# Optimization experiments

Measured on AMD Instinct MI355X. Metric: run time of the kernel, lower is better.

The kernel has to match this reference:

```python
import jax, jax.numpy as jnp
import numpy as np

B, T, C = 8, 2048, 1024
NEG_BIG = -1e30  # exp(NEG_BIG - row_max) underflows to exactly 0 in fp32


def setup_inputs() -> dict:
    key = jax.random.key(0)
    k1, k2 = jax.random.split(key)
    x = jax.random.normal(k1, (B, T, C), dtype=jnp.float32)
    # nn.Linear weight, shape [out, in]; forward computes x @ W^T
    W_H = jax.random.normal(k2, (C, C), dtype=jnp.float32) * (1.0 / np.sqrt(C))
    return {"x": x, "W_H": W_H}


def reference(x, W_H):
    Tdim = x.shape[1]
    xH = jnp.einsum('btc,dc->btd', x, W_H)          # H(x) = x @ W^T, [B,T,C]
    scores = jnp.einsum('btc,bsc->bts', x, xH)       # bilinear scores, [B,T,T]
    # tril_plus_one=True -> strictly-lower-triangular mask (diagonal=-1)
    mask = jnp.tril(jnp.ones((Tdim, Tdim), dtype=bool), k=-1)
    scores = jnp.where(mask, scores, NEG_BIG)
    wei = jax.nn.softmax(scores, axis=-1)            # fully-masked rows -> uniform, zeroed below
    all_masked = ~mask.any(axis=-1)                  # [T], True for row 0
    wei = jnp.where(all_masked[None, :, None], 0.0, wei)
    out = jnp.einsum('bts,bsc->btc', wei, xH)
    return -out
```

## Files before the change

### kernel.cpp

```cpp
#include <hip/hip_runtime.h>
#include <stdint.h>

#define Bn 8
#define Tn 2048
#define Cn 1024
#define Mn (Bn * Tn)
#define NTRI 136
#define NLIN2 72

typedef __attribute__((ext_vector_type(4))) float f32x4;
typedef _Float16 f16;
typedef __attribute__((ext_vector_type(8))) _Float16 f16x8;
typedef uint16_t u16;
typedef uint32_t u32;

static __device__ __forceinline__ u16 f2h(float f) {
  union { f16 h; u16 u; } c; c.h = (f16)f; return c.u;
}
static __device__ __forceinline__ f32x4 mfmaH(f16x8 a, f16x8 b, f32x4 c) {
  return __builtin_amdgcn_mfma_f32_16x16x32_f16(a, b, c, 0, 0, 0);
}
static __device__ __forceinline__ void gld16(const void* g, void* l) {
  __builtin_amdgcn_global_load_lds(
      (const __attribute__((address_space(1))) u32*)g,
      (__attribute__((address_space(3))) u32*)l, 16, 0, 0);
}

__global__ __launch_bounds__(256) void ksplitW(const float* __restrict__ s,
                                               u16* __restrict__ hi) {
  size_t i = ((size_t)blockIdx.x * 256 + threadIdx.x) * 8;
  float4 a = *(const float4*)(s + i), b = *(const float4*)(s + i + 4);
  float f[8] = {a.x, a.y, a.z, a.w, b.x, b.y, b.z, b.w};
  union { u16 u[8]; uint4 v; } H;
#pragma unroll
  for (int j = 0; j < 8; ++j) H.u[j] = f2h(f[j]);
  *(uint4*)(hi + i) = H.v;
}

__global__ __launch_bounds__(256) void ksplitX(const float* __restrict__ s,
                                               u16* __restrict__ hi,
                                               u16* __restrict__ lo) {
  size_t i = ((size_t)blockIdx.x * 256 + threadIdx.x) * 8;
  float4 a = *(const float4*)(s + i), b = *(const float4*)(s + i + 4);
  float f[8] = {a.x, a.y, a.z, a.w, b.x, b.y, b.z, b.w};
  union { u16 u[8]; uint4 v; } H, L;
#pragma unroll
  for (int j = 0; j < 8; ++j) {
    f16 h = (f16)f[j];
    union { f16 h; u16 u; } ch; ch.h = h;
    H.u[j] = ch.u;
    L.u[j] = f2h(f[j] - (float)h);
  }
  *(uint4*)(hi + i) = H.v;
  *(uint4*)(lo + i) = L.v;
}

__global__ __launch_bounds__(256) void k1_xh(const u16* __restrict__ x_h,
                                             const u16* __restrict__ W_h,
                                             u16* __restrict__ xh) {
  __shared__ __align__(16) u16 Ah[8192], Bh[8192];
  const int tid = threadIdx.x;
  const int m0 = blockIdx.x * 128, n0 = blockIdx.y * 128;
  const int wave = tid >> 6, lane = tid & 63;
  const int wrow = (wave >> 1) * 64, wcol = (wave & 1) * 64;
  const int quad = lane >> 4, l16 = lane & 15;

  f32x4 acc[4][4] = {};

  for (int k0 = 0; k0 < Cn; k0 += 64) {
#pragma unroll
    for (int i = 0; i < 4; ++i) {
      int chunk = i * 256 + tid;
      int kk = chunk >> 9, row = (chunk >> 2) & 127, c8 = (chunk & 3) * 8;
      gld16(x_h + (size_t)(m0 + row) * Cn + k0 + kk * 32 + c8, Ah + chunk * 8);
      gld16(W_h + (size_t)(n0 + row) * Cn + k0 + kk * 32 + c8, Bh + chunk * 8);
    }
    __syncthreads();
#pragma unroll
    for (int kk = 0; kk < 2; ++kk) {
      f16x8 a[4], b[4];
#pragma unroll
      for (int i = 0; i < 4; ++i) {
        a[i] = *(const f16x8*)(Ah + kk * 4096 + (wrow + i * 16 + l16) * 32 + quad * 8);
        b[i] = *(const f16x8*)(Bh + kk * 4096 + (wcol + i * 16 + l16) * 32 + quad * 8);
      }
#pragma unroll
      for (int mi = 0; mi < 4; ++mi)
#pragma unroll
        for (int ni = 0; ni < 4; ++ni)
          acc[mi][ni] = mfmaH(a[mi], b[ni], acc[mi][ni]);
    }
    __syncthreads();
  }
#pragma unroll
  for (int mi = 0; mi < 4; ++mi)
#pragma unroll
    for (int ni = 0; ni < 4; ++ni)
#pragma unroll
      for (int r = 0; r < 4; ++r) {
        int row = wrow + mi * 16 + quad * 4 + r;
        int col = wcol + ni * 16 + l16;
        xh[(size_t)(m0 + row) * Cn + n0 + col] = f2h(acc[mi][ni][r]);
      }
}

__global__ __launch_bounds__(512) void k2_scores(const u16* __restrict__ x_h,
                                                 const u16* __restrict__ x_l,
                                                 const u16* __restrict__ xh,
                                                 u16* __restrict__ P,
                                                 float* __restrict__ mt,
                                                 float* __restrict__ lt) {
  __shared__ __align__(16) union {
    struct { u16 Ah[3][4096], Al[3][4096], Bh[3][8192]; } s;
    struct { float Mrow[4][128]; float Lrow[4][128]; } e;
  } u;
  const int tid = threadIdx.x;
  const int bL = blockIdx.y;
  const int lin = blockIdx.x;
  int qt = 0, cum = 0;
  while (cum + ((qt >> 1) + 1) <= lin) { cum += (qt >> 1) + 1; qt++; }
  const int bcol = lin - cum;
  const int t0 = qt * 128, s0 = bcol * 256;
  const int wave = tid >> 6, lane = tid & 63;
  const int wc = wave & 3;
  const int wrow = (wave >> 2) * 64, wcol = wc * 64;
  const int quad = lane >> 4, l16 = lane & 15;

  f32x4 acc[4][4] = {};
  const size_t abase = ((size_t)bL * Tn + t0) * Cn;
  const size_t bbase = ((size_t)bL * Tn + s0) * Cn;
  const int arow = tid >> 2, ac8 = (tid & 3) * 8;

  auto stage = [&](int buf, int k0) {
    size_t aoff = abase + (size_t)arow * Cn + k0 + ac8;
    gld16(x_h + aoff, &u.s.Ah[buf][tid * 8]);
    gld16(x_l + aoff, &u.s.Al[buf][tid * 8]);
#pragma unroll
    for (int i = 0; i < 2; ++i) {
      int ch = i * 512 + tid;
      int row = ch >> 2, c8 = (ch & 3) * 8;
      gld16(xh + bbase + (size_t)row * Cn + k0 + c8, &u.s.Bh[buf][ch * 8]);
    }
  };

  stage(0, 0);
  stage(1, 32);
  int cur = 0;
#pragma unroll 1
  for (int kidx = 0; kidx < 32; ++kidx) {
    if (kidx < 31) {
      asm volatile("s_waitcnt vmcnt(4) lgkmcnt(0)" ::: "memory");
    } else {
      asm volatile("s_waitcnt vmcnt(0) lgkmcnt(0)" ::: "memory");
    }
    __builtin_amdgcn_s_barrier();
    __builtin_amdgcn_sched_barrier(0);
    if (kidx < 30) {
      int tgt = cur >= 1 ? cur - 1 : 2;
      stage(tgt, (kidx + 2) * 32);
    }
    f16x8 b[4];
#pragma unroll
    for (int ni = 0; ni < 4; ++ni)
      b[ni] = *(const f16x8*)&u.s.Bh[cur][(wcol + ni * 16 + l16) * 32 + quad * 8];
#pragma unroll
    for (int mi = 0; mi < 4; ++mi) {
      f16x8 ah = *(const f16x8*)&u.s.Ah[cur][(wrow + mi * 16 + l16) * 32 + quad * 8];
      f16x8 al = *(const f16x8*)&u.s.Al[cur][(wrow + mi * 16 + l16) * 32 + quad * 8];
#pragma unroll
      for (int ni = 0; ni < 4; ++ni) {
        acc[mi][ni] = mfmaH(ah, b[ni], acc[mi][ni]);
        acc[mi][ni] = mfmaH(al, b[ni], acc[mi][ni]);
      }
    }
    cur = cur < 2 ? cur + 1 : 0;
  }

  float rm[4][4];
#pragma unroll
  for (int mi = 0; mi < 4; ++mi)
#pragma unroll
    for (int r = 0; r < 4; ++r) {
      int row = wrow + mi * 16 + quad * 4 + r;
      float m = -1e30f;
#pragma unroll
      for (int ni = 0; ni < 4; ++ni) {
        int scol = s0 + wcol + ni * 16 + l16;
        if (scol >= t0 + row) acc[mi][ni][r] = -1e30f;
        m = fmaxf(m, acc[mi][ni][r]);
      }
      m = fmaxf(m, __shfl_xor(m, 1));
      m = fmaxf(m, __shfl_xor(m, 2));
      m = fmaxf(m, __shfl_xor(m, 4));
      m = fmaxf(m, __shfl_xor(m, 8));
      rm[mi][r] = m;
    }
  if (l16 == 0) {
#pragma unroll
    for (int mi = 0; mi < 4; ++mi)
#pragma unroll
      for (int r = 0; r < 4; ++r)
        u.e.Mrow[wc][wrow + mi * 16 + quad * 4 + r] = rm[mi][r];
  }
  __syncthreads();
  const int h2 = (wc >> 1) * 2;
  float rs[4][4];
#pragma unroll
  for (int mi = 0; mi < 4; ++mi)
#pragma unroll
    for (int r = 0; r < 4; ++r) {
      int row = wrow + mi * 16 + quad * 4 + r;
      float m2 = fmaxf(u.e.Mrow[h2][row], u.e.Mrow[h2 + 1][row]);
      float s = 0.f;
#pragma unroll
      for (int ni = 0; ni < 4; ++ni) {
        int scol = s0 + wcol + ni * 16 + l16;
        float p = (scol < t0 + row) ? __expf(acc[mi][ni][r] - m2) : 0.0f;
        acc[mi][ni][r] = p;
        s += p;
      }
      s += __shfl_xor(s, 1);
      s += __shfl_xor(s, 2);
      s += __shfl_xor(s, 4);
      s += __shfl_xor(s, 8);
      rs[mi][r] = s;
      rm[mi][r] = m2;
    }
  if (l16 == 0) {
#pragma unroll
    for (int mi = 0; mi < 4; ++mi)
#pragma unroll
      for (int r = 0; r < 4; ++r)
        u.e.Lrow[wc][wrow + mi * 16 + quad * 4 + r] = rs[mi][r];
  }
  __syncthreads();
  const int st128 = bcol * 2 + (wc >> 1);
  if (st128 <= qt) {
    if ((wc & 1) == 0 && l16 == 0) {
#pragma unroll
      for (int mi = 0; mi < 4; ++mi)
#pragma unroll
        for (int r = 0; r < 4; ++r) {
          int row = wrow + mi * 16 + quad * 4 + r;
          size_t rI = (size_t)bL * Tn + t0 + row;
          mt[rI * 16 + st128] = rm[mi][r];
          lt[rI * 16 + st128] = u.e.Lrow[wc][row] + u.e.Lrow[wc + 1][row];
        }
    }
    const size_t pbase = (size_t)(bL * NTRI + qt * (qt + 1) / 2 + st128) * 16384;
#pragma unroll
    for (int mi = 0; mi < 4; ++mi)
#pragma unroll
      for (int ni = 0; ni < 4; ++ni)
#pragma unroll
        for (int r = 0; r < 4; ++r) {
          int row = wrow + mi * 16 + quad * 4 + r;
          int pcol = (wcol & 64) + ni * 16 + l16;
          P[pbase + row * 128 + pcol] = f2h(acc[mi][ni][r]);
        }
  }
}

__global__ __launch_bounds__(256) void k3_stats(const float* __restrict__ mt,
                                                const float* __restrict__ lt,
                                                float* __restrict__ Mr,
                                                float* __restrict__ Li) {
  int r = blockIdx.x * 256 + threadIdx.x;
  int t = r & (Tn - 1);
  int nt = (t == 0) ? 0 : (((t - 1) >> 7) + 1);
  float M = -1e30f;
  for (int i = 0; i < nt; ++i) M = fmaxf(M, mt[(size_t)r * 16 + i]);
  float L = 0.f;
  for (int i = 0; i < nt; ++i) L += lt[(size_t)r * 16 + i] * __expf(mt[(size_t)r * 16 + i] - M);
  Mr[r] = M;
  Li[r] = (L > 0.f) ? 1.f / L : 0.f;
}

__global__ __launch_bounds__(256) void ktr(const u16* __restrict__ src,
                                           u16* __restrict__ dst) {
  __shared__ __align__(16) u16 S[128 * 136];
  const int t0 = blockIdx.x * 128, c0 = blockIdx.y * 128, b = blockIdx.z;
  const int tid = threadIdx.x;
#pragma unroll
  for (int i = 0; i < 8; ++i) {
    int chunk = tid + i * 256;
    int row = chunk >> 4, c8 = (chunk & 15) * 8;
    uint4 v = *(const uint4*)(src + ((size_t)b * Tn + t0 + row) * Cn + c0 + c8);
    *(uint4*)(S + row * 136 + c8) = v;
  }
  __syncthreads();
#pragma unroll
  for (int i = 0; i < 8; ++i) {
    int chunk = tid + i * 256;
    int crow = chunk >> 4, t8 = (chunk & 15) * 8;
    union { u16 s[8]; uint4 v; } o;
#pragma unroll
    for (int j = 0; j < 8; ++j) o.s[j] = S[(t8 + j) * 136 + crow];
    *(uint4*)(dst + ((size_t)b * Cn + c0 + crow) * Tn + t0 + t8) = o.v;
  }
}

__global__ __launch_bounds__(512) void k4_out(const u16* __restrict__ P,
                                              const u16* __restrict__ xhT,
                                              const float* __restrict__ mt,
                                              const float* __restrict__ Mr,
                                              const float* __restrict__ Li,
                                              float* __restrict__ out) {
  __shared__ __align__(16) u16 Ap[3][4096], Bp[3][8192];
  __shared__ u16 alphaLds[16 * 128];
  const int tid = threadIdx.x;
  const int tt = 15 - blockIdx.x;
  const int cn = blockIdx.y, bL = blockIdx.z;
  const int t0 = tt * 128, c0 = cn * 256;
  const int wave = tid >> 6, lane = tid & 63;
  const int wc = wave & 3;
  const int wrow = (wave >> 2) * 64, wcol = wc * 64;
  const int quad = lane >> 4, l16 = lane & 15;

  {
    const size_t rbase = (size_t)bL * Tn + t0;
#pragma unroll
    for (int j = 0; j < 4; ++j) {
      int idx = tid + j * 512;
      int stp = idx >> 7, row = idx & 127;
      float a = 0.f;
      if (stp <= tt)
        a = __expf(mt[(rbase + row) * 16 + stp] - Mr[rbase + row]) * Li[rbase + row];
      alphaLds[idx] = f2h(a);
    }
  }

  f32x4 acc[4][4] = {};
  const size_t bbase = ((size_t)bL * Cn + c0) * Tn;
  const size_t ptile0 = (size_t)(bL * NTRI + tt * (tt + 1) / 2) * 16384;

  auto stage = [&](int buf, int step) {
    const int st = step >> 2, k32 = (step & 3) * 32;
    {
      int row = tid >> 2, c8 = (tid & 3) * 8;
      gld16(P + ptile0 + (size_t)st * 16384 + row * 128 + k32 + c8,
            &Ap[buf][tid * 8]);
    }
#pragma unroll
    for (int i = 0; i < 2; ++i) {
      int ch = i * 512 + tid;
      int row = ch >> 2, c8 = (ch & 3) * 8;
      gld16(xhT + bbase + (size_t)row * Tn + st * 128 + k32 + c8,
            &Bp[buf][ch * 8]);
    }
  };

  const int steps = 4 * (tt + 1);
  stage(0, 0);
  stage(1, 1);
  int cur = 0;
#pragma unroll 1
  for (int s = 0; s < steps; ++s) {
    if (s < steps - 1) {
      asm volatile("s_waitcnt vmcnt(3) lgkmcnt(0)" ::: "memory");
    } else {
      asm volatile("s_waitcnt vmcnt(0) lgkmcnt(0)" ::: "memory");
    }
    __builtin_amdgcn_s_barrier();
    __builtin_amdgcn_sched_barrier(0);
    if (s < steps - 2) {
      int tgt = cur >= 1 ? cur - 1 : 2;
      stage(tgt, s + 2);
    }
    const int st = s >> 2;
    f16x8 b[4];
#pragma unroll
    for (int ni = 0; ni < 4; ++ni)
      b[ni] = *(const f16x8*)&Bp[cur][(wcol + ni * 16 + l16) * 32 + quad * 8];
#pragma unroll
    for (int mi = 0; mi < 4; ++mi) {
      union { u16 u; f16 h; } ca;
      ca.u = alphaLds[st * 128 + wrow + mi * 16 + l16];
      f16x8 sv;
#pragma unroll
      for (int j = 0; j < 8; ++j) sv[j] = ca.h;
      f16x8 a = *(const f16x8*)&Ap[cur][(wrow + mi * 16 + l16) * 32 + quad * 8];
      a = a * sv;
#pragma unroll
      for (int ni = 0; ni < 4; ++ni)
        acc[mi][ni] = mfmaH(a, b[ni], acc[mi][ni]);
    }
    cur = cur < 2 ? cur + 1 : 0;
  }

#pragma unroll
  for (int mi = 0; mi < 4; ++mi)
#pragma unroll
    for (int ni = 0; ni < 4; ++ni)
#pragma unroll
      for (int r = 0; r < 4; ++r) {
        int row = wrow + mi * 16 + quad * 4 + r;
        int col = wcol + ni * 16 + l16;
        out[((size_t)bL * Tn + t0 + row) * Cn + c0 + col] = -acc[mi][ni][r];
      }
}

extern "C" void kernel_launch(void* const* d_in, const int* in_sizes, int n_in,
                              void* d_out, int out_size, void* d_ws, size_t ws_size,
                              hipStream_t stream) {
  (void)in_sizes; (void)n_in; (void)out_size;
  const float* x = (const float*)d_in[0];
  const float* W = (const float*)d_in[1];
  float* out = (float*)d_out;

  const size_t FULL_NEED = 3ull * Mn * Cn * 2 + (size_t)Bn * NTRI * 16384 * 2 +
                           (size_t)Cn * Cn * 2 + 2ull * Mn * 16 * 4 + 2ull * Mn * 4;
  const int nch = (ws_size >= FULL_NEED) ? 1 : 2;
  const int nb = Bn / nch;
  const size_t rowsC = (size_t)nb * Tn;
  const size_t sA = rowsC * Cn * 2;

  char* p = (char*)d_ws;
  u16* x_h = (u16*)p; p += sA;
  u16* xLT = (u16*)p; p += sA;
  u16* xh  = (u16*)p; p += sA;
  u16* Pp  = (u16*)p; p += (size_t)nb * NTRI * 16384 * 2;
  u16* W_h = (u16*)p; p += (size_t)Cn * Cn * 2;
  float* mt = (float*)p; p += rowsC * 16 * 4;
  float* lt = (float*)p; p += rowsC * 16 * 4;
  float* Mr = (float*)p; p += rowsC * 4;
  float* Li = (float*)p; p += rowsC * 4;

  dim3 blk(256);
  ksplitW<<<dim3(Cn * Cn / 2048), blk, 0, stream>>>(W, W_h);
  for (int c = 0; c < nch; ++c) {
    const float* xc = x + (size_t)c * rowsC * Cn;
    float* oc = out + (size_t)c * rowsC * Cn;
    ksplitX<<<dim3((u32)(rowsC * Cn / 2048)), blk, 0, stream>>>(xc, x_h, xLT);
    k1_xh<<<dim3((u32)(rowsC / 128), Cn / 128), blk, 0, stream>>>(x_h, W_h, xh);
    k2_scores<<<dim3(NLIN2, nb), dim3(512), 0, stream>>>(x_h, xLT, xh, Pp, mt, lt);
    k3_stats<<<dim3((u32)(rowsC / 256)), blk, 0, stream>>>(mt, lt, Mr, Li);
    ktr<<<dim3(Tn / 128, Cn / 128, nb), blk, 0, stream>>>(xh, xLT);
    k4_out<<<dim3(16, Cn / 256, nb), dim3(512), 0, stream>>>(Pp, xLT, mt, Mr, Li, oc);
  }
}
```

Measured before the change: 384.6 us.

## Remap score blocks per XCD column and switch to double-buffered LDS

The scores kernel now uses a 1D grid and remaps block IDs so that each XCD (bid & 7) handles a fixed pair of key columns (c and 7-c) for a subset of batches. Blocks sharing the same key tile therefore land on the same L2, and the load per XCD is balanced across the triangular tile set. The LDS pipeline also drops from triple to double buffering. The next stage is issued only after a second barrier that follows the MFMA work, which cuts LDS use but reduces how far prefetch can run ahead of compute.

```diff
diff --git a/kernel.cpp b/kernel.cpp
--- a/kernel.cpp
+++ b/kernel.cpp
@@ -6,7 +6,6 @@
 #define Cn 1024
 #define Mn (Bn * Tn)
 #define NTRI 136
-#define NLIN2 72
 
 typedef __attribute__((ext_vector_type(4))) float f32x4;
 typedef _Float16 f16;
@@ -111,16 +110,26 @@
                                                  float* __restrict__ mt,
                                                  float* __restrict__ lt) {
   __shared__ __align__(16) union {
-    struct { u16 Ah[3][4096], Al[3][4096], Bh[3][8192]; } s;
+    struct { u16 Ah[2][4096], Al[2][4096], Bh[2][8192]; } s;
     struct { float Mrow[4][128]; float Lrow[4][128]; } e;
   } u;
   const int tid = threadIdx.x;
-  const int bL = blockIdx.y;
-  const int lin = blockIdx.x;
-  int qt = 0, cum = 0;
-  while (cum + ((qt >> 1) + 1) <= lin) { cum += (qt >> 1) + 1; qt++; }
-  const int bcol = lin - cum;
+
+  const int bid = blockIdx.x;
+  const int half = gridDim.x / 144;
+  const int xcd = bid & 7, slot = bid >> 3;
+  const int p = xcd & 3, h = xcd >> 2;
+  const int n1 = 16 - 2 * p, n2 = 2 * p + 2;
+  int c, j, bb;
+  if (slot < n1 * half) {
+    c = p; bb = slot / n1; j = slot % n1;
+  } else {
+    int s2 = slot - n1 * half; c = 7 - p; bb = s2 / n2; j = s2 % n2;
+  }
+  const int bL = h * half + bb;
+  const int qt = 2 * c + j, bcol = c;
   const int t0 = qt * 128, s0 = bcol * 256;
+
   const int wave = tid >> 6, lane = tid & 63;
   const int wc = wave & 3;
   const int wrow = (wave >> 2) * 64, wcol = wc * 64;
@@ -145,20 +154,16 @@
 
   stage(0, 0);
   stage(1, 32);
-  int cur = 0;
 #pragma unroll 1
   for (int kidx = 0; kidx < 32; ++kidx) {
     if (kidx < 31) {
-      asm volatile("s_waitcnt vmcnt(4) lgkmcnt(0)" ::: "memory");
+      asm volatile("s_waitcnt vmcnt(4)" ::: "memory");
     } else {
-      asm volatile("s_waitcnt vmcnt(0) lgkmcnt(0)" ::: "memory");
+      asm volatile("s_waitcnt vmcnt(0)" ::: "memory");
     }
     __builtin_amdgcn_s_barrier();
     __builtin_amdgcn_sched_barrier(0);
-    if (kidx < 30) {
-      int tgt = cur >= 1 ? cur - 1 : 2;
-      stage(tgt, (kidx + 2) * 32);
-    }
+    const int cur = kidx & 1;
     f16x8 b[4];
 #pragma unroll
     for (int ni = 0; ni < 4; ++ni)
@@ -173,7 +178,10 @@
         acc[mi][ni] = mfmaH(al, b[ni], acc[mi][ni]);
       }
     }
-    cur = cur < 2 ? cur + 1 : 0;
+    asm volatile("s_waitcnt lgkmcnt(0)" ::: "memory");
+    __builtin_amdgcn_sched_barrier(0);
+    __builtin_amdgcn_s_barrier();
+    if (kidx < 30) stage(cur, (kidx + 2) * 32);
   }
 
   float rm[4][4];
@@ -215,9 +223,9 @@
 #pragma unroll
       for (int ni = 0; ni < 4; ++ni) {
         int scol = s0 + wcol + ni * 16 + l16;
-        float p = (scol < t0 + row) ? __expf(acc[mi][ni][r] - m2) : 0.0f;
-        acc[mi][ni][r] = p;
-        s += p;
+        float pv = (scol < t0 + row) ? __expf(acc[mi][ni][r] - m2) : 0.0f;
+        acc[mi][ni][r] = pv;
+        s += pv;
       }
       s += __shfl_xor(s, 1);
       s += __shfl_xor(s, 2);
@@ -433,7 +441,7 @@
     float* oc = out + (size_t)c * rowsC * Cn;
     ksplitX<<<dim3((u32)(rowsC * Cn / 2048)), blk, 0, stream>>>(xc, x_h, xLT);
     k1_xh<<<dim3((u32)(rowsC / 128), Cn / 128), blk, 0, stream>>>(x_h, W_h, xh);
-    k2_scores<<<dim3(NLIN2, nb), dim3(512), 0, stream>>>(x_h, xLT, xh, Pp, mt, lt);
+    k2_scores<<<dim3(72 * nb), dim3(512), 0, stream>>>(x_h, xLT, xh, Pp, mt, lt);
     k3_stats<<<dim3((u32)(rowsC / 256)), blk, 0, stream>>>(mt, lt, Mr, Li);
     ktr<<<dim3(Tn / 128, Cn / 128, nb), blk, 0, stream>>>(xh, xLT);
     k4_out<<<dim3(16, Cn / 256, nb), dim3(512), 0, stream>>>(Pp, xLT, mt, Mr, Li, oc);
```

Measured after the change: 385.9 us. About the same (+0.3%).
